# Kernel optimization log

Hardware: AMD Instinct MI355X
Metric: run time of the kernel (lower is better)

## Reference

```python
import jax, jax.numpy as jnp
import numpy as np

EMBEDDING_BOUND = 1e4  # uniform init bound for box centers (repo constant)


def setup_inputs() -> dict:
    key = jax.random.key(0)
    k1, k2, k3 = jax.random.split(key, 3)
    num_classes, dim = 100000, 50
    d = dim // 2
    # init per MultiBoxEL.init_embeddings: centers ~ U(-B, B), offsets ~ N(1, 0.333)
    centers = jax.random.uniform(k1, (num_classes, d), dtype=jnp.float32,
                                 minval=-EMBEDDING_BOUND, maxval=EMBEDDING_BOUND)
    offsets = 1.0 + 0.333 * jax.random.normal(k2, (num_classes, d), dtype=jnp.float32)
    class_embeds = jnp.concatenate([centers, offsets], axis=1)  # [C, dim]
    nf1_data = jax.random.randint(k3, (2_000_000, 2), 0, num_classes)  # [N, 2] class ids
    return {"class_embeds": class_embeds, "nf1_data": nf1_data}


def _to_box(emb):
    # get_multiboxes: first half = center, second half = |offsets|
    d = emb.shape[-1] // 2
    return emb[:, :d], jnp.abs(emb[:, d:])


def reference(class_embeds, nf1_data):
    """nf1_loss (C subsumed-by D): batched inclusion loss 1 - Area(C ^ D)/Area(C),
    then L2 norm of relu(losses) over the batch (a scalar), exactly as inclusion_loss."""
    c_emb = class_embeds[nf1_data[:, 0]]  # [N, dim] gather (memory-bound)
    d_emb = class_embeds[nf1_data[:, 1]]
    cc, co = _to_box(c_emb)
    dc, do = _to_box(d_emb)
    # box intersection: [max(lowers), min(uppers)]; empty -> side length clipped to 0
    lo = jnp.maximum(cc - co, dc - do)
    hi = jnp.minimum(cc + co, dc + do)
    inter_area = jnp.prod(jax.nn.relu(hi - lo), axis=-1)  # [N]
    c_area = jnp.prod(2.0 * co, axis=-1)                  # [N] box volume = prod(2*offset)
    loss = jnp.where(c_area == 0, 0.0,
           jnp.where(jnp.isinf(c_area), 1.0 - inter_area / (2.0 * EMBEDDING_BOUND),
                     1.0 - inter_area / c_area))
    return jnp.linalg.norm(jax.nn.relu(loss))
```

## Files before the change

kernel.cpp:

```cpp
#include <hip/hip_runtime.h>
#include <math.h>


#define DIMS 25
#define EMB_BOUND 10000.0f
#define FBLK 1024
#define TROWS 128
#define TFLOATS (TROWS * 2 * DIMS)

__global__ void init_ws_kernel(float* ws) {
    if (threadIdx.x == 0 && blockIdx.x == 0) ws[0] = 0.0f;
}

__global__ __launch_bounds__(256, 8) void nf1_fallback_kernel(
    const float* __restrict__ emb, const int2* __restrict__ pairs,
    int n_pairs, float* __restrict__ ws)
{
    const int gl  = threadIdx.x & 31;
    const int gid = blockIdx.x * (blockDim.x >> 5) + (threadIdx.x >> 5);
    const int ngrp = gridDim.x * (blockDim.x >> 5);
    float acc = 0.0f;
    for (int p = gid; p < n_pairs; p += ngrp) {
        int2 pr = pairs[p];
        const float* rc = emb + (size_t)pr.x * (2 * DIMS);
        const float* rd = emb + (size_t)pr.y * (2 * DIMS);
        float t = 1.0f, a = 1.0f;
        if (gl < DIMS) {
            float cc = rc[gl], co = fabsf(rc[DIMS + gl]);
            float dc = rd[gl], dd = fabsf(rd[DIMS + gl]);
            float lo = fmaxf(cc - co, dc - dd);
            float hi = fminf(cc + co, dc + dd);
            t = fmaxf(hi - lo, 0.0f);
            a = 2.0f * co;
        }
        #pragma unroll
        for (int m = 16; m >= 1; m >>= 1) { t *= __shfl_xor(t, m, 32); a *= __shfl_xor(a, m, 32); }
        float loss;
        if (a == 0.0f)     loss = 0.0f;
        else if (isinf(a)) loss = 1.0f - t / (2.0f * EMB_BOUND);
        else               loss = 1.0f - t / a;
        loss = fmaxf(loss, 0.0f);
        if (gl == 0) acc += loss * loss;
    }
    #pragma unroll
    for (int m = 32; m >= 1; m >>= 1) acc += __shfl_xor(acc, m, 64);
    __shared__ float wsum[4];
    if ((threadIdx.x & 63) == 0) wsum[threadIdx.x >> 6] = acc;
    __syncthreads();
    if (threadIdx.x == 0) atomicAdd(ws, wsum[0] + wsum[1] + wsum[2] + wsum[3]);
}

__global__ void fallback_finalize_kernel(const float* __restrict__ ws, float* __restrict__ out) {
    if (threadIdx.x == 0 && blockIdx.x == 0) out[0] = sqrtf(fmaxf(ws[0], 0.0f));
}

__device__ __forceinline__ float slow_pair(const float* __restrict__ emb, int2 pr) {
    const float* ra = emb + (size_t)pr.x * (2 * DIMS);
    const float* rb = emb + (size_t)pr.y * (2 * DIMS);
    float inter = 1.0f, carea = 1.0f;
    for (int j = 0; j < DIMS; j++) {
        float cc = ra[j], co = fabsf(ra[DIMS + j]);
        float dc = rb[j], dd = fabsf(rb[DIMS + j]);
        float lo = fmaxf(cc - co, dc - dd);
        float hi = fminf(cc + co, dc + dd);
        inter *= fmaxf(hi - lo, 0.0f);
        carea *= 2.0f * co;
    }
    float loss;
    if (carea == 0.0f)     loss = 0.0f;
    else if (isinf(carea)) loss = 1.0f - inter / (2.0f * EMB_BOUND);
    else                   loss = 1.0f - inter / carea;
    loss = fmaxf(loss, 0.0f);
    return loss * loss;
}

__device__ __forceinline__ float key_pair(const float2* __restrict__ keys,
                                          const float* __restrict__ emb, int2 pr) {
    float2 ka = keys[pr.x];
    float2 kb = keys[pr.y];
    float t0 = fminf(ka.y, kb.y) - fmaxf(ka.x, kb.x);
    if (t0 > 0.0f) return slow_pair(emb, pr);
    return 1.0f;
}

template <int K>
__device__ __forceinline__ int ring_bucket(float lo, float hi) {
    float w = hi - lo;
    if (w <= 16.0f && fabsf(lo) <= 1.0e6f) {
        int i = (int)floorf(lo * 0.0625f);
        int b = i % K; if (b < 0) b += K;
        return b;
    }
    return K;
}

__device__ __forceinline__ bool ring_pass(unsigned a, unsigned b, unsigned K) {
    unsigned dd = (a >= b) ? (a - b) : (b - a);
    return (a == K) | (b == K) | (dd <= 1u) | (dd == K - 1u);
}

__global__ __launch_bounds__(256) void repack_tile_kernel(
    const float* __restrict__ emb, float2* __restrict__ keys,
    unsigned char* __restrict__ gbuck, int n_rows,
    float* __restrict__ acc, unsigned* __restrict__ ticket)
{
    __shared__ float tile[TFLOATS];
    if (blockIdx.x == 0 && threadIdx.x == 0) { acc[0] = 0.0f; ticket[0] = 0u; }
    const int n_tiles = (n_rows + TROWS - 1) / TROWS;
    for (int tIdx = blockIdx.x; tIdx < n_tiles; tIdx += gridDim.x) {
        const int r0 = tIdx * TROWS;
        const int rows = min(TROWS, n_rows - r0);
        const int cnt = rows * (2 * DIMS);
        const int n4 = cnt >> 2;
        {
            const float4* g4 = (const float4*)(emb + (size_t)r0 * (2 * DIMS));
            float4* s4 = (float4*)tile;
            for (int i = threadIdx.x; i < n4; i += blockDim.x) s4[i] = g4[i];
            for (int i = (n4 << 2) + threadIdx.x; i < cnt; i += blockDim.x)
                tile[i] = emb[(size_t)r0 * (2 * DIMS) + i];
        }
        __syncthreads();
        for (int j = threadIdx.x; j < rows; j += blockDim.x) {
            float c = tile[j * (2 * DIMS)];
            float o = fabsf(tile[j * (2 * DIMS) + DIMS]);
            float lo = c - o, hi = c + o;
            keys[r0 + j] = make_float2(lo, hi);
            gbuck[r0 + j] = (unsigned char)ring_bucket<255>(lo, hi);
        }
        __syncthreads();
    }
}

__global__ __launch_bounds__(FBLK, 1) void screen_byte_kernel(
    const float2* __restrict__ keys, const unsigned char* __restrict__ gbuck,
    const float* __restrict__ emb, const int2* __restrict__ pairs,
    int n_pairs, int n_rows, float* __restrict__ acc,
    unsigned* __restrict__ ticket, float* __restrict__ out)
{
    extern __shared__ unsigned char sbuck[];
    __shared__ float wsum[FBLK / 64];
    const int nthreads = gridDim.x * blockDim.x;
    const int t = blockIdx.x * blockDim.x + threadIdx.x;
    const int noct = n_pairs >> 3;
    const int4* p4 = (const int4*)pairs;

    int4 qa, qb, qc, qd;
    const bool have0 = t < noct;
    if (have0) {
        qa = p4[4 * t + 0]; qb = p4[4 * t + 1];
        qc = p4[4 * t + 2]; qd = p4[4 * t + 3];
    }

    {
        const int nb16 = (n_rows + 15) >> 4;
        const uint4* g4 = (const uint4*)gbuck;
        uint4* s4 = (uint4*)sbuck;
        for (int i = threadIdx.x; i < nb16; i += blockDim.x) s4[i] = g4[i];
    }
    __syncthreads();

    float sum = 0.0f;
    for (int q = t; q < noct; q += nthreads) {
        if (q != t) {
            qa = p4[4 * q + 0]; qb = p4[4 * q + 1];
            qc = p4[4 * q + 2]; qd = p4[4 * q + 3];
        }
        int2 pr[8] = { make_int2(qa.x, qa.y), make_int2(qa.z, qa.w),
                       make_int2(qb.x, qb.y), make_int2(qb.z, qb.w),
                       make_int2(qc.x, qc.y), make_int2(qc.z, qc.w),
                       make_int2(qd.x, qd.y), make_int2(qd.z, qd.w) };
        unsigned ba[8], bb[8];
        #pragma unroll
        for (int i = 0; i < 8; i++) { ba[i] = sbuck[pr[i].x]; bb[i] = sbuck[pr[i].y]; }
        #pragma unroll
        for (int i = 0; i < 8; i++) {
            if (ring_pass(ba[i], bb[i], 255u)) sum += key_pair(keys, emb, pr[i]);
            else                               sum += 1.0f;
        }
    }
    for (int p = (noct << 3) + t; p < n_pairs; p += nthreads) {
        int2 pr = pairs[p];
        unsigned a = sbuck[pr.x], b = sbuck[pr.y];
        if (ring_pass(a, b, 255u)) sum += key_pair(keys, emb, pr);
        else                       sum += 1.0f;
    }

    #pragma unroll
    for (int m = 32; m >= 1; m >>= 1) sum += __shfl_xor(sum, m, 64);
    if ((threadIdx.x & 63) == 0) wsum[threadIdx.x >> 6] = sum;
    __syncthreads();
    if (threadIdx.x == 0) {
        float s = 0.0f;
        #pragma unroll
        for (int w = 0; w < FBLK / 64; w++) s += wsum[w];
        atomicAdd(acc, s);
        __threadfence();
        unsigned tk = atomicAdd(ticket, 1u);
        if (tk == gridDim.x - 1)
            out[0] = sqrtf(fmaxf(atomicAdd(acc, 0.0f), 0.0f));
    }
}

extern "C" void kernel_launch(void* const* d_in, const int* in_sizes, int n_in,
                              void* d_out, int out_size, void* d_ws, size_t ws_size,
                              hipStream_t stream) {
    const float* emb  = (const float*)d_in[0];
    const int2*  prs  = (const int2*)d_in[1];
    int n_pairs = in_sizes[1] / 2;
    int n_rows  = in_sizes[0] / (2 * DIMS);

    float*    ws     = (float*)d_ws;
    unsigned* ticket = (unsigned*)(ws + 1);
    float*    out    = (float*)d_out;
    float2*   keys   = (float2*)((char*)d_ws + 256);
    unsigned char* gbuck = (unsigned char*)(keys + n_rows);

    int dev = 0;  hipGetDevice(&dev);
    int maxShared = 0;
    hipDeviceGetAttribute(&maxShared, hipDeviceAttributeMaxSharedMemoryPerBlock, dev);

    const size_t tabBytes = (size_t)((n_rows + 15) & ~15);
    const bool ws_ok = (ws_size >= 256 + (size_t)n_rows * 8 + tabBytes + 64) &&
                       ((n_rows & 1) == 0);
    const bool byte_ok = ((size_t)maxShared >= tabBytes + 512) && ws_ok;

    if (byte_ok) {
        const int n_tiles = (n_rows + TROWS - 1) / TROWS;
        hipLaunchKernelGGL(repack_tile_kernel, dim3(min(n_tiles, 2048)), dim3(256),
                           0, stream, emb, keys, gbuck, n_rows, ws, ticket);
        hipLaunchKernelGGL(screen_byte_kernel, dim3(256), dim3(FBLK),
                           tabBytes, stream,
                           keys, gbuck, emb, prs, n_pairs, n_rows, ws, ticket, out);
    } else {
        hipLaunchKernelGGL(init_ws_kernel, dim3(1), dim3(64), 0, stream, ws);
        hipLaunchKernelGGL(nf1_fallback_kernel, dim3(4096), dim3(256), 0, stream,
                           emb, prs, n_pairs, ws);
        hipLaunchKernelGGL(fallback_finalize_kernel, dim3(1), dim3(64), 0, stream, ws, out);
    }
}
```

Baseline: 87.59 us.

## Fuse repack and screening kernels into one cooperative launch with grid sync

Combines the per-row key/bucket repack and the pair screening pass into a single cooperative kernel, with a grid-wide barrier between the phases. The first octet of pair indices is prefetched before the barrier, and the host-side device attribute queries are replaced by a hard-coded shared-memory limit. This removes one kernel launch and its boundary gap. In exchange, the repack phase runs on only 256 blocks of 1024 threads, and the grid sync adds a barrier cost.

```diff
diff --git a/kernel.cpp b/kernel.cpp
--- a/kernel.cpp
+++ b/kernel.cpp
@@ -1,10 +1,15 @@
 #include <hip/hip_runtime.h>
+#include <hip/hip_cooperative_groups.h>
 #include <math.h>
+
+namespace cg = cooperative_groups;
 
 
 #define DIMS 25
 #define EMB_BOUND 10000.0f
 #define FBLK 1024
+#define FTROWS 256
+#define TILE_BYTES (FTROWS * 2 * DIMS * 4)
 #define TROWS 128
 #define TFLOATS (TROWS * 2 * DIMS)
 
@@ -99,6 +104,106 @@
     return (a == K) | (b == K) | (dd <= 1u) | (dd == K - 1u);
 }
 
+__global__ __launch_bounds__(FBLK, 1) void fused3_kernel(
+    const float* __restrict__ emb, float2* __restrict__ keys,
+    unsigned char* __restrict__ gbuck, const int2* __restrict__ pairs,
+    int n_pairs, int n_rows, float* __restrict__ acc,
+    unsigned* __restrict__ ticket, float* __restrict__ out)
+{
+    extern __shared__ unsigned char smem[];
+    __shared__ float wsum[FBLK / 64];
+    const int nthreads = gridDim.x * blockDim.x;
+    const int t = blockIdx.x * blockDim.x + threadIdx.x;
+    if (t == 0) { acc[0] = 0.0f; ticket[0] = 0u; }
+
+    {
+        float* tile = (float*)smem;
+        const int n_tiles = (n_rows + FTROWS - 1) / FTROWS;
+        for (int tIdx = blockIdx.x; tIdx < n_tiles; tIdx += gridDim.x) {
+            const int r0 = tIdx * FTROWS;
+            const int rows = min(FTROWS, n_rows - r0);
+            const int cnt = rows * (2 * DIMS);
+            const int n4 = cnt >> 2;
+            {
+                const float4* g4 = (const float4*)(emb + (size_t)r0 * (2 * DIMS));
+                float4* s4 = (float4*)tile;
+                for (int i = threadIdx.x; i < n4; i += blockDim.x) s4[i] = g4[i];
+                for (int i = (n4 << 2) + threadIdx.x; i < cnt; i += blockDim.x)
+                    tile[i] = emb[(size_t)r0 * (2 * DIMS) + i];
+            }
+            __syncthreads();
+            for (int j = threadIdx.x; j < rows; j += blockDim.x) {
+                float c = tile[j * (2 * DIMS)];
+                float o = fabsf(tile[j * (2 * DIMS) + DIMS]);
+                float lo = c - o, hi = c + o;
+                keys[r0 + j] = make_float2(lo, hi);
+                gbuck[r0 + j] = (unsigned char)ring_bucket<255>(lo, hi);
+            }
+            __syncthreads();
+        }
+    }
+
+    const int noct = n_pairs >> 3;
+    const int4* p4 = (const int4*)pairs;
+    int4 qa, qb, qc, qd;
+    if (t < noct) {
+        qa = p4[4 * t + 0]; qb = p4[4 * t + 1];
+        qc = p4[4 * t + 2]; qd = p4[4 * t + 3];
+    }
+
+    cg::this_grid().sync();
+
+    unsigned char* sbuck = smem;
+    {
+        const int nb16 = (n_rows + 15) >> 4;
+        const uint4* g4 = (const uint4*)gbuck;
+        uint4* s4 = (uint4*)sbuck;
+        for (int i = threadIdx.x; i < nb16; i += blockDim.x) s4[i] = g4[i];
+    }
+    __syncthreads();
+
+    float sum = 0.0f;
+    for (int q = t; q < noct; q += nthreads) {
+        if (q != t) {
+            qa = p4[4 * q + 0]; qb = p4[4 * q + 1];
+            qc = p4[4 * q + 2]; qd = p4[4 * q + 3];
+        }
+        int2 pr[8] = { make_int2(qa.x, qa.y), make_int2(qa.z, qa.w),
+                       make_int2(qb.x, qb.y), make_int2(qb.z, qb.w),
+                       make_int2(qc.x, qc.y), make_int2(qc.z, qc.w),
+                       make_int2(qd.x, qd.y), make_int2(qd.z, qd.w) };
+        unsigned ba[8], bb[8];
+        #pragma unroll
+        for (int i = 0; i < 8; i++) { ba[i] = sbuck[pr[i].x]; bb[i] = sbuck[pr[i].y]; }
+        #pragma unroll
+        for (int i = 0; i < 8; i++) {
+            if (ring_pass(ba[i], bb[i], 255u)) sum += key_pair(keys, emb, pr[i]);
+            else                               sum += 1.0f;
+        }
+    }
+    for (int p = (noct << 3) + t; p < n_pairs; p += nthreads) {
+        int2 pr = pairs[p];
+        unsigned a = sbuck[pr.x], b = sbuck[pr.y];
+        if (ring_pass(a, b, 255u)) sum += key_pair(keys, emb, pr);
+        else                       sum += 1.0f;
+    }
+
+    #pragma unroll
+    for (int m = 32; m >= 1; m >>= 1) sum += __shfl_xor(sum, m, 64);
+    if ((threadIdx.x & 63) == 0) wsum[threadIdx.x >> 6] = sum;
+    __syncthreads();
+    if (threadIdx.x == 0) {
+        float s = 0.0f;
+        #pragma unroll
+        for (int w = 0; w < FBLK / 64; w++) s += wsum[w];
+        atomicAdd(acc, s);
+        __threadfence();
+        unsigned tk = atomicAdd(ticket, 1u);
+        if (tk == gridDim.x - 1)
+            out[0] = sqrtf(fmaxf(atomicAdd(acc, 0.0f), 0.0f));
+    }
+}
+
 __global__ __launch_bounds__(256) void repack_tile_kernel(
     const float* __restrict__ emb, float2* __restrict__ keys,
     unsigned char* __restrict__ gbuck, int n_rows,
@@ -145,12 +250,10 @@
     const int4* p4 = (const int4*)pairs;
 
     int4 qa, qb, qc, qd;
-    const bool have0 = t < noct;
-    if (have0) {
+    if (t < noct) {
         qa = p4[4 * t + 0]; qb = p4[4 * t + 1];
         qc = p4[4 * t + 2]; qd = p4[4 * t + 3];
     }
-
     {
         const int nb16 = (n_rows + 15) >> 4;
         const uint4* g4 = (const uint4*)gbuck;
@@ -215,23 +318,35 @@
     float2*   keys   = (float2*)((char*)d_ws + 256);
     unsigned char* gbuck = (unsigned char*)(keys + n_rows);
 
-    int dev = 0;  hipGetDevice(&dev);
-    int maxShared = 0;
-    hipDeviceGetAttribute(&maxShared, hipDeviceAttributeMaxSharedMemoryPerBlock, dev);
-
     const size_t tabBytes = (size_t)((n_rows + 15) & ~15);
+    const size_t fusedDyn = tabBytes > (size_t)TILE_BYTES ? tabBytes
+                                                          : (size_t)TILE_BYTES;
     const bool ws_ok = (ws_size >= 256 + (size_t)n_rows * 8 + tabBytes + 64) &&
                        ((n_rows & 1) == 0);
-    const bool byte_ok = ((size_t)maxShared >= tabBytes + 512) && ws_ok;
-
-    if (byte_ok) {
+    const bool byte_ok = ws_ok && (tabBytes + 512 <= 160 * 1024);
+
+    bool launched = false;
+    if (byte_ok && (fusedDyn + 512 <= 160 * 1024)) {
+        void* args[] = { (void*)&emb, (void*)&keys, (void*)&gbuck,
+                         (void*)&prs, (void*)&n_pairs, (void*)&n_rows,
+                         (void*)&ws, (void*)&ticket, (void*)&out };
+        hipError_t le = hipLaunchCooperativeKernel(
+            (const void*)fused3_kernel, dim3(256), dim3(FBLK),
+            args, (unsigned int)fusedDyn, stream);
+        if (le == hipSuccess) launched = true;
+    }
+
+    if (!launched && byte_ok) {
         const int n_tiles = (n_rows + TROWS - 1) / TROWS;
         hipLaunchKernelGGL(repack_tile_kernel, dim3(min(n_tiles, 2048)), dim3(256),
                            0, stream, emb, keys, gbuck, n_rows, ws, ticket);
         hipLaunchKernelGGL(screen_byte_kernel, dim3(256), dim3(FBLK),
                            tabBytes, stream,
                            keys, gbuck, emb, prs, n_pairs, n_rows, ws, ticket, out);
-    } else {
+        launched = true;
+    }
+
+    if (!launched) {
         hipLaunchKernelGGL(init_ws_kernel, dim3(1), dim3(64), 0, stream, ws);
         hipLaunchKernelGGL(nf1_fallback_kernel, dim3(4096), dim3(256), 0, stream,
                            emb, prs, n_pairs, ws);
```

Result: slower. 140.1 us (+59.9%).
